# Kernel tuning notes

Measured on AMD Instinct MI355X. Metric: run time of the kernel, lower is better.

## Reference

```python
import jax, jax.numpy as jnp
import numpy as np

NEG = -1e9

def conv1x1(x, w, b):
    # x: [B,C,H,W], w: [O,C], b: [O]
    return jnp.einsum('bchw,oc->bohw', x, w) + b[None, :, None, None]


def setup_inputs() -> dict:
    key = jax.random.key(0)
    ks = jax.random.split(key, 12)
    B, C, H, W = 4, 512, 96, 96
    Cr = min(8, C // 8)  # = 8
    s = lambda fan: 1.0 / np.sqrt(fan)
    inp = {
        'x':   jax.random.normal(ks[0], (B, C, H, W), dtype=jnp.float32),
        'w_h': jax.random.normal(ks[1], (Cr, C), dtype=jnp.float32) * s(C),
        'b_h': jax.random.normal(ks[2], (Cr,), dtype=jnp.float32) * s(C),
        'w_w': jax.random.normal(ks[3], (Cr, C), dtype=jnp.float32) * s(C),
        'b_w': jax.random.normal(ks[4], (Cr,), dtype=jnp.float32) * s(C),
        'w_c': jax.random.normal(ks[5], (C, C), dtype=jnp.float32) * s(C),
        'b_c': jax.random.normal(ks[6], (C,), dtype=jnp.float32) * s(C),
        'w_o': jax.random.normal(ks[7], (C, C), dtype=jnp.float32) * s(C),
        'b_o': jax.random.normal(ks[8], (C,), dtype=jnp.float32) * s(C),
        # alpha/beta/gamma are nn.Parameter(zeros(1)); use small nonzero values
        # so all branches contribute to output/gradients.
        'alpha': jax.random.normal(ks[9], (1,), dtype=jnp.float32) * 0.1,
        'beta':  jax.random.normal(ks[10], (1,), dtype=jnp.float32) * 0.1,
        'gamma': jax.random.normal(ks[11], (1,), dtype=jnp.float32) * 0.1,
    }
    return inp


def reference(x, w_h, b_h, w_w, b_w, w_c, b_c, w_o, b_o, alpha, beta, gamma):
    B, C, H, W = x.shape
    f_hei = conv1x1(x, w_h, b_h)              # [B,Cr,H,W]
    Cr = f_hei.shape[1]
    # Faithful replication of torch permute/contiguous/view sequence
    # (the .view(B*W,-1,H) after permute reinterprets the (H,Cr) layout as (Cr,H)).
    f_h = f_hei.transpose(0, 3, 2, 1).reshape(B * W, Cr, H).transpose(0, 2, 1)  # [B*W,H,Cr]
    f_w = f_hei.transpose(0, 2, 1, 3).reshape(B * H, Cr, W).transpose(0, 2, 1)  # [B*H,W,Cr]
    f_wid = conv1x1(x, w_w, b_w)              # [B,Cr,H,W]
    ff_h = f_wid.transpose(0, 3, 1, 2).reshape(B * W, Cr, H)  # [B*W,Cr,H]
    ff_w = f_wid.transpose(0, 2, 1, 3).reshape(B * H, Cr, W)  # [B*H,Cr,W]
    # channel attention branch
    f_ch = conv1x1(x, w_c, b_c)               # [B,C,H,W]
    f_c = f_ch.reshape(B, C, H * W)           # [B,C,HW]
    ff_c = f_ch.transpose(0, 2, 3, 1).reshape(B, H * W, C)    # [B,HW,C]
    aff_c = jax.nn.softmax(jnp.matmul(f_c, ff_c), axis=2)     # [B,C,C]
    out_C = jnp.matmul(ff_c, aff_c).reshape(B, C, H, W)       # torch .view reinterpretation
    # axial (criss-cross) attention with masked concat-softmax
    E_h = jnp.matmul(f_h, ff_h)               # [B*W,H,H]
    E_h = E_h + (jnp.eye(H, dtype=x.dtype) * NEG)[None, :, :]
    E_h = E_h.reshape(B, W, H, H).transpose(0, 2, 1, 3)       # [B,H,W,H]
    E_w = jnp.matmul(f_w, ff_w).reshape(B, H, W, W)           # [B,H,W,W]
    concate = jax.nn.softmax(jnp.concatenate([E_h, E_w], axis=3), axis=3)  # [B,H,W,H+W]
    h_att = concate[:, :, :, :H].transpose(0, 2, 1, 3).reshape(B * W, H, H)
    w_att = concate[:, :, :, H:].reshape(B * H, W, W)
    f_cha = conv1x1(x, w_o, b_o)              # [B,C,H,W]
    P_H = f_cha.transpose(0, 3, 1, 2).reshape(B * W, C, H)
    P_W = f_cha.transpose(0, 2, 1, 3).reshape(B * H, C, W)
    out_H = jnp.matmul(P_H, h_att.transpose(0, 2, 1)).reshape(B, W, C, H).transpose(0, 2, 3, 1)
    out_W = jnp.matmul(P_W, w_att.transpose(0, 2, 1)).reshape(B, H, C, W).transpose(0, 2, 1, 3)
    return x + alpha * out_H + beta * out_W + gamma * out_C
```

## Files before the change

### kernel.cpp

```cpp
#include <hip/hip_runtime.h>

typedef __attribute__((ext_vector_type(8))) short short8;
typedef __attribute__((ext_vector_type(4))) float f32x4;
typedef __attribute__((ext_vector_type(4))) unsigned short us4;
typedef unsigned short u16;

#define kB 4
#define kC 512
#define kCr 8
#define kH 96
#define kW 96
#define kHW 9216
#define kCHW 4718592
#define NEGV -1e9f

__device__ __forceinline__ u16 f2b(float f) {
  union { float f; unsigned u; } v; v.f = f;
  unsigned r = v.u + 0x7fff + ((v.u >> 16) & 1);
  return (u16)(r >> 16);
}
__device__ __forceinline__ float b2f(u16 h) {
  union { unsigned u; float f; } v; v.u = ((unsigned)h) << 16;
  return v.f;
}
#define MFMA(a, b, c) __builtin_amdgcn_mfma_f32_16x16x32_bf16(a, b, c, 0, 0, 0)

__device__ __forceinline__ void gl16(const u16* g, u16* l) {
  __builtin_amdgcn_global_load_lds(
      (const __attribute__((address_space(1))) void*)g,
      (__attribute__((address_space(3))) void*)l, 16, 0, 0);
}

__global__ __launch_bounds__(256) void k_cvt_T(const float* __restrict__ in,
                                               u16* __restrict__ out,
                                               int R, int C) {
  const float* ib = in + (size_t)blockIdx.z * R * C;
  u16* ob = out + (size_t)blockIdx.z * R * C;
  int c0 = blockIdx.x * 64, r0 = blockIdx.y * 64;
  __shared__ u16 T[64][68];
  int tid = threadIdx.x;
#pragma unroll
  for (int p = 0; p < 4; p++) {
    int ch = tid + p * 256;
    int i = ch >> 4, seg = ch & 15;
    f32x4 v = *(const f32x4*)&ib[(size_t)(r0 + i) * C + c0 + seg * 4];
    T[i][seg*4+0] = f2b(v[0]); T[i][seg*4+1] = f2b(v[1]);
    T[i][seg*4+2] = f2b(v[2]); T[i][seg*4+3] = f2b(v[3]);
  }
  __syncthreads();
#pragma unroll
  for (int p = 0; p < 4; p++) {
    int ch = tid + p * 256;
    int j = ch >> 4, seg = ch & 15;
    us4 o;
#pragma unroll
    for (int e = 0; e < 4; e++) o[e] = T[seg*4+e][j];
    *(us4*)&ob[(size_t)(c0 + j) * R + r0 + seg * 4] = o;
  }
}

__global__ __launch_bounds__(256) void k_cvtw(const float* __restrict__ wc,
                                              const float* __restrict__ wo,
                                              u16* __restrict__ wco) {
  int i = blockIdx.x * 256 + threadIdx.x;
  const float* src = (i < 65536) ? &wc[(size_t)i * 4] : &wo[(size_t)(i - 65536) * 4];
  f32x4 v = *(const f32x4*)src;
  us4 o;
  o[0] = f2b(v[0]); o[1] = f2b(v[1]); o[2] = f2b(v[2]); o[3] = f2b(v[3]);
  ((us4*)wco)[i] = o;
}

__global__ __launch_bounds__(256) void k_conv16(
    const float* __restrict__ wh, const float* __restrict__ bh,
    const float* __restrict__ ww, const float* __restrict__ bw,
    const u16* __restrict__ XT, u16* __restrict__ Out) {
  __shared__ u16 As[16][520];
  __shared__ float bias_s[16];
  int tid = threadIdx.x;
#pragma unroll
  for (int p = 0; p < 4; p++) {
    int ch = tid + p * 256;
    int r = ch >> 6, seg = ch & 63;
    const float* src = (r < 8) ? &wh[r * 512 + seg * 8] : &ww[(r - 8) * 512 + seg * 8];
    f32x4 v0 = *(const f32x4*)src;
    f32x4 v1 = *(const f32x4*)(src + 4);
    short8 sv;
    sv[0]=f2b(v0[0]); sv[1]=f2b(v0[1]); sv[2]=f2b(v0[2]); sv[3]=f2b(v0[3]);
    sv[4]=f2b(v1[0]); sv[5]=f2b(v1[1]); sv[6]=f2b(v1[2]); sv[7]=f2b(v1[3]);
    *(short8*)&As[r][seg * 8] = sv;
  }
  if (tid < 16) bias_s[tid] = (tid < 8) ? bh[tid] : bw[tid - 8];
  __syncthreads();
  int b = blockIdx.y;
  int nb = blockIdx.x * 128 + (tid >> 6) * 32;
  int lane = tid & 63;
  int lr = lane & 15, lg = lane >> 4;
  const u16* Bb = XT + (size_t)b * kCHW;
  f32x4 acc[2] = {};
#pragma unroll 4
  for (int k0 = 0; k0 < 512; k0 += 32) {
    short8 a = *(const short8*)&As[lr][k0 + lg * 8];
    short8 b0 = *(const short8*)&Bb[(size_t)(nb + lr) * 512 + k0 + lg * 8];
    short8 b1 = *(const short8*)&Bb[(size_t)(nb + 16 + lr) * 512 + k0 + lg * 8];
    acc[0] = MFMA(a, b0, acc[0]);
    acc[1] = MFMA(a, b1, acc[1]);
  }
#pragma unroll
  for (int q = 0; q < 2; q++)
#pragma unroll
    for (int r = 0; r < 4; r++) {
      int m = lg * 4 + r;
      Out[((size_t)b * 16 + m) * kHW + nb + q * 16 + lr] = f2b(acc[q][r] + bias_s[m]);
    }
}

#define GEMM_PROLOG()                                                      \
  int tid = threadIdx.x;                                                   \
  int lane = tid & 63, wv = tid >> 6;                                      \
  int wr = (wv >> 1) * 64, wc = (wv & 1) * 64;                             \
  int lr = lane & 15, lg = lane >> 4;                                      \
  f32x4 acc[4][4] = {};

#define STAGE(bufv, kk)                                                    \
  {                                                                        \
    _Pragma("unroll")                                                      \
    for (int p = 0; p < 4; p++) {                                          \
      int ch = tid + p * 256;                                              \
      int row = ch >> 3, cc = ch & 7;                                      \
      int sc = (cc ^ (row & 7)) * 8;                                       \
      gl16(&Asrc[(size_t)(bm + row) * LDA + (kk) + sc], &As[bufv][row][cc * 8]); \
      gl16(&Bsrc[(size_t)(bn + row) * LDB + (kk) + sc], &Bs[bufv][row][cc * 8]); \
    }                                                                      \
  }

#define COMPUTE(bufv)                                                      \
  {                                                                        \
    _Pragma("unroll")                                                      \
    for (int ks = 0; ks < 2; ks++) {                                       \
      int ca = ((ks * 4 + lg) ^ (lr & 7)) * 8;                             \
      short8 av[4], bv[4];                                                 \
      _Pragma("unroll")                                                    \
      for (int m = 0; m < 4; m++)                                          \
        av[m] = *(const short8*)&As[bufv][wr + m * 16 + lr][ca];           \
      _Pragma("unroll")                                                    \
      for (int n = 0; n < 4; n++)                                          \
        bv[n] = *(const short8*)&Bs[bufv][wc + n * 16 + lr][ca];           \
      __builtin_amdgcn_s_setprio(1);                                       \
      _Pragma("unroll")                                                    \
      for (int m = 0; m < 4; m++)                                          \
        _Pragma("unroll")                                                  \
        for (int n = 0; n < 4; n++)                                        \
          acc[m][n] = MFMA(av[m], bv[n], acc[m][n]);                       \
      __builtin_amdgcn_s_setprio(0);                                       \
    }                                                                      \
  }

#define VMBAR(N)                                                           \
  asm volatile("s_waitcnt vmcnt(" #N ")" ::: "memory");                    \
  __builtin_amdgcn_s_barrier();

#define LGBAR                                                              \
  asm volatile("s_waitcnt lgkmcnt(0)" ::: "memory");                       \
  __builtin_amdgcn_s_barrier();

#define PIPELOOP(NT, KBASE)                                                \
  STAGE(0, (KBASE));                                                       \
  STAGE(1, (KBASE) + 64);                                                  \
  {                                                                        \
    int cur = 0;                                                           \
    _Pragma("unroll 1")                                                    \
    for (int t = 0; t < (NT) - 2; t++) {                                   \
      VMBAR(8);                                                            \
      COMPUTE(cur);                                                        \
      LGBAR;                                                               \
      STAGE(cur, (KBASE) + (t + 2) * 64);                                  \
      cur ^= 1;                                                            \
    }                                                                      \
    VMBAR(8);                                                              \
    COMPUTE(cur);                                                          \
    cur ^= 1;                                                              \
    VMBAR(0);                                                              \
    COMPUTE(cur);                                                          \
  }

__global__ __launch_bounds__(256) void k_gemm_conv2(
    const u16* __restrict__ wco, const u16* __restrict__ BT,
    const float* __restrict__ b_c, const float* __restrict__ b_o,
    u16* __restrict__ f_ch, u16* __restrict__ f_cha, u16* __restrict__ f_chT) {
  __shared__ u16 smem[32768];
  u16 (*As)[128][64] = (u16 (*)[128][64])smem;
  u16 (*Bs)[128][64] = (u16 (*)[128][64])(smem + 16384);
  int b = blockIdx.z;
  int bm = blockIdx.y * 128;
  int bn = blockIdx.x * 128;
  const u16* Asrc = wco;
  const u16* Bsrc = BT + (size_t)b * kCHW;
  const int LDA = 512, LDB = 512;
  GEMM_PROLOG();
  PIPELOOP(8, 0);
  const float* biasp = (bm < 512) ? (b_c + bm) : (b_o + bm - 512);
  u16* Ob = (bm < 512) ? (f_ch + (size_t)b * kCHW + (size_t)bm * kHW)
                       : (f_cha + (size_t)b * kCHW + (size_t)(bm - 512) * kHW);
  u16 tvals[4][4];
#pragma unroll
  for (int m = 0; m < 4; m++)
#pragma unroll
    for (int r = 0; r < 4; r++) {
      int ol = wr + m * 16 + lg * 4 + r;
      float bv_ = biasp[ol];
#pragma unroll
      for (int n = 0; n < 4; n++) {
        u16 hv = f2b(acc[m][n][r] + bv_);
        Ob[(size_t)ol * kHW + bn + wc + n * 16 + lr] = hv;
        tvals[m][n] = (r == 0) ? hv : tvals[m][n];
      }
    }
  if (bm < 512) {
    __syncthreads();
    u16 (*T)[136] = (u16 (*)[136])smem;
#pragma unroll
    for (int m = 0; m < 4; m++)
#pragma unroll
      for (int n = 0; n < 4; n++) {
        int ol = wr + m * 16 + lg * 4;
        float bv0 = biasp[ol], bv1 = biasp[ol+1], bv2 = biasp[ol+2], bv3 = biasp[ol+3];
        int nl = wc + n * 16 + lr;
        T[nl][ol + 0] = f2b(acc[m][n][0] + bv0);
        T[nl][ol + 1] = f2b(acc[m][n][1] + bv1);
        T[nl][ol + 2] = f2b(acc[m][n][2] + bv2);
        T[nl][ol + 3] = f2b(acc[m][n][3] + bv3);
      }
    __syncthreads();
    u16* Tb = f_chT + (size_t)b * kCHW;
#pragma unroll
    for (int p = 0; p < 16; p++) {
      int ch = tid + p * 256;
      int row = ch >> 5, seg = ch & 31;
      us4 v = *(const us4*)&T[row][seg * 4];
      *(us4*)&Tb[(size_t)(bn + row) * 512 + bm + seg * 4] = v;
    }
  }
}

__global__ __launch_bounds__(256) void k_gram_sk(const u16* __restrict__ F,
                                                 u16* __restrict__ part) {
  __shared__ u16 As[2][128][64];
  __shared__ u16 Bs[2][128][64];
  int z = blockIdx.z;
  int b = z & 3, s = z >> 2;
  int L = blockIdx.x;
  int bm = (int)((0x3221110000ull >> (4 * L)) & 15) * 128;
  int bn = (int)((0x3323213210ull >> (4 * L)) & 15) * 128;
  const u16* Asrc = F + (size_t)b * kCHW;
  const u16* Bsrc = Asrc;
  const int LDA = kHW, LDB = kHW;
  int kbeg = s * 1152;
  GEMM_PROLOG();
  PIPELOOP(18, kbeg);
  u16* Pb = part + ((size_t)(s * 4 + b)) * 262144;
#pragma unroll
  for (int m = 0; m < 4; m++)
#pragma unroll
    for (int n = 0; n < 4; n++) {
      us4 tv;
#pragma unroll
      for (int r = 0; r < 4; r++) {
        tv[r] = f2b(acc[m][n][r]);
        Pb[(size_t)(bm + wr + m * 16 + lg * 4 + r) * 512 + bn + wc + n * 16 + lr] = tv[r];
      }
      if (bm != bn)
        *(us4*)&Pb[(size_t)(bn + wc + n * 16 + lr) * 512 + bm + wr + m * 16 + lg * 4] = tv;
    }
}

__global__ __launch_bounds__(256) void k_outc(
    const u16* __restrict__ AT, const u16* __restrict__ Bt,
    const float* __restrict__ gamma, u16* __restrict__ Out) {
  __shared__ u16 As[2][128][64];
  __shared__ u16 Bs[2][128][64];
  int b = blockIdx.z;
  int bm = blockIdx.y * 128;
  int bn = blockIdx.x * 128;
  const u16* Asrc = AT + (size_t)b * kCHW;
  const u16* Bsrc = Bt + (size_t)b * 262144;
  const int LDA = 512, LDB = 512;
  GEMM_PROLOG();
  PIPELOOP(8, 0);
  float g = *gamma;
  u16* Ob = Out + (size_t)b * kCHW;
#pragma unroll
  for (int m = 0; m < 4; m++)
#pragma unroll
    for (int r = 0; r < 4; r++) {
      int mm = bm + wr + m * 16 + lg * 4 + r;
#pragma unroll
      for (int n = 0; n < 4; n++)
        Ob[(size_t)mm * 512 + bn + wc + n * 16 + lr] = f2b(g * acc[m][n][r]);
    }
}

__global__ __launch_bounds__(256) void k_softmax512r(const u16* __restrict__ part,
                                                     float* __restrict__ gramN) {
  int b = blockIdx.x >> 9, i = blockIdx.x & 511;
  int tid = threadIdx.x;
  float v0 = 0.f, v1 = 0.f;
#pragma unroll
  for (int s = 0; s < 8; s++) {
    const u16* P = part + ((size_t)(s * 4 + b) * 512 + i) * 512;
    v0 += b2f(P[tid]);
    v1 += b2f(P[tid + 256]);
  }
  int wid = tid >> 6, lane = tid & 63;
  float m = fmaxf(v0, v1);
#pragma unroll
  for (int o = 32; o >= 1; o >>= 1) m = fmaxf(m, __shfl_xor(m, o));
  __shared__ float redm[4], reds[4];
  if (lane == 0) redm[wid] = m;
  __syncthreads();
  m = fmaxf(fmaxf(redm[0], redm[1]), fmaxf(redm[2], redm[3]));
  float e0 = expf(v0 - m), e1 = expf(v1 - m);
  float s = e0 + e1;
#pragma unroll
  for (int o = 32; o >= 1; o >>= 1) s += __shfl_xor(s, o);
  if (lane == 0) reds[wid] = s;
  __syncthreads();
  s = reds[0] + reds[1] + reds[2] + reds[3];
  float inv = 1.0f / s;
  float* R = gramN + ((size_t)b * 512 + i) * 512;
  R[tid] = e0 * inv;
  R[tid + 256] = e1 * inv;
}

__global__ __launch_bounds__(256) void k_eh(
    const u16* __restrict__ fhw, u16* __restrict__ Ccat) {
  int b = blockIdx.x / kW, w = blockIdx.x % kW;
  __shared__ float fh[kH][kCr];
  __shared__ float fw[kCr][kH];
  int tid = threadIdx.x;
  for (int l = tid; l < kH * kCr; l += 256) {
    int i = l >> 3, c = l & 7;
    fh[i][c] = b2f(fhw[((size_t)b * 16 + (i & 7)) * kHW + (c * 12 + (i >> 3)) * kW + w]);
    int c2 = l / kH, j = l % kH;
    fw[c2][j] = b2f(fhw[((size_t)b * 16 + 8 + c2) * kHW + j * kW + w]);
  }
  __syncthreads();
  for (int t = tid; t < kH * kH; t += 256) {
    int i = t / kH, j = t % kH;
    float e = 0.f;
#pragma unroll
    for (int c = 0; c < kCr; c++) e += fh[i][c] * fw[c][j];
    if (i == j) e += NEGV;
    Ccat[(((size_t)b * kH + i) * kW + w) * 192 + j] = f2b(e);
  }
}

__global__ __launch_bounds__(256) void k_ew(
    const u16* __restrict__ fhw, u16* __restrict__ Ccat) {
  int b = blockIdx.x / kH, h = blockIdx.x % kH;
  __shared__ float fh2[kCr][kW];
  __shared__ float fw2[kCr][kW];
  int tid = threadIdx.x;
  for (int l = tid; l < kCr * kW; l += 256) {
    int c = l / kW, w = l % kW;
    fh2[c][w] = b2f(fhw[((size_t)b * 16 + c) * kHW + h * kW + w]);
    fw2[c][w] = b2f(fhw[((size_t)b * 16 + 8 + c) * kHW + h * kW + w]);
  }
  __syncthreads();
  for (int t = tid; t < kW * kW; t += 256) {
    int w = t / kW, j = t % kW;
    float e = 0.f;
#pragma unroll
    for (int c = 0; c < kCr; c++) e += fh2[c][w] * fw2[c][j];
    Ccat[(((size_t)b * kH + h) * kW + w) * 192 + 96 + j] = f2b(e);
  }
}

__global__ __launch_bounds__(256) void k_softmax192(u16* __restrict__ Ccat) {
  int r = blockIdx.x * 4 + (threadIdx.x >> 6);
  int lane = threadIdx.x & 63;
  u16* R = Ccat + (size_t)r * 192;
  float a = b2f(R[lane]), b = b2f(R[lane + 64]), c = b2f(R[lane + 128]);
  float m = fmaxf(a, fmaxf(b, c));
#pragma unroll
  for (int o = 32; o >= 1; o >>= 1) m = fmaxf(m, __shfl_xor(m, o));
  float ea = expf(a - m), eb = expf(b - m), ec = expf(c - m);
  float s = ea + eb + ec;
#pragma unroll
  for (int o = 32; o >= 1; o >>= 1) s += __shfl_xor(s, o);
  float inv = 1.0f / s;
  R[lane] = f2b(ea * inv);
  R[lane + 64] = f2b(eb * inv);
  R[lane + 128] = f2b(ec * inv);
}

__global__ __launch_bounds__(256) void k_tr_plane(const u16* __restrict__ in,
                                                  u16* __restrict__ out) {
  size_t pl = blockIdx.x;
  const u16* ib = in + pl * 9216;
  u16* ob = out + pl * 9216;
  __shared__ u16 T[96][100];
  int tid = threadIdx.x;
  for (int ch = tid; ch < 96 * 24; ch += 256) {
    int i = ch / 24, seg = ch % 24;
    *(us4*)&T[i][seg*4] = *(const us4*)&ib[i*96 + seg*4];
  }
  __syncthreads();
  for (int ch = tid; ch < 96 * 24; ch += 256) {
    int j = ch / 24, seg = ch % 24;
    us4 o;
#pragma unroll
    for (int e = 0; e < 4; e++) o[e] = T[seg*4+e][j];
    *(us4*)&ob[j*96 + seg*4] = o;
  }
}

__global__ __launch_bounds__(512) void k_final_h(
    const u16* __restrict__ AT,
    const u16* __restrict__ att,
    const float* __restrict__ alpha,
    u16* __restrict__ OutHT) {
  int b = blockIdx.x / 96, w = blockIdx.x % 96;
  __shared__ u16 Bs[96][104];
  int tid = threadIdx.x;
  for (int ch = tid; ch < 1152; ch += 512) {
    int h = ch / 12, seg = ch % 12;
    *(short8*)&Bs[h][seg*8] =
        *(const short8*)&att[(((size_t)b*96 + h)*96 + w)*192 + seg*8];
  }
  __syncthreads();
  int lane = tid & 63, wv = tid >> 6;
  int lr = lane & 15, lg = lane >> 4;
  int c0 = wv * 64;
  const u16* Ab = AT + ((size_t)b*512 + c0)*kHW + w*96;
  f32x4 acc[4][6] = {};
#pragma unroll
  for (int ks = 0; ks < 3; ks++) {
    short8 av[4];
#pragma unroll
    for (int m = 0; m < 4; m++)
      av[m] = *(const short8*)&Ab[(size_t)(m*16 + lr)*kHW + ks*32 + lg*8];
#pragma unroll
    for (int n = 0; n < 6; n++) {
      short8 bv = *(const short8*)&Bs[n*16 + lr][ks*32 + lg*8];
#pragma unroll
      for (int m = 0; m < 4; m++) acc[m][n] = MFMA(av[m], bv, acc[m][n]);
    }
  }
  float al = *alpha;
  u16* Ob = OutHT + ((size_t)b*512 + c0)*kHW + w*96;
#pragma unroll
  for (int m = 0; m < 4; m++)
#pragma unroll
    for (int r = 0; r < 4; r++) {
      size_t crow = (size_t)(m*16 + lg*4 + r) * kHW;
#pragma unroll
      for (int n = 0; n < 6; n++)
        Ob[crow + n*16 + lr] = f2b(al * acc[m][n][r]);
    }
}

__global__ __launch_bounds__(512) void k_final_w(
    const u16* __restrict__ A,
    const u16* __restrict__ att,
    const float* __restrict__ beta,
    u16* __restrict__ OutW) {
  int b = blockIdx.x / 96, h = blockIdx.x % 96;
  __shared__ u16 Bs[96][104];
  int tid = threadIdx.x;
  for (int ch = tid; ch < 1152; ch += 512) {
    int wr_ = ch / 12, seg = ch % 12;
    *(short8*)&Bs[wr_][seg*8] =
        *(const short8*)&att[(((size_t)b*96 + h)*96 + wr_)*192 + 96 + seg*8];
  }
  __syncthreads();
  int lane = tid & 63, wv = tid >> 6;
  int lr = lane & 15, lg = lane >> 4;
  int c0 = wv * 64;
  const u16* Ab = A + ((size_t)b*512 + c0)*kHW + h*96;
  f32x4 acc[4][6] = {};
#pragma unroll
  for (int ks = 0; ks < 3; ks++) {
    short8 av[4];
#pragma unroll
    for (int m = 0; m < 4; m++)
      av[m] = *(const short8*)&Ab[(size_t)(m*16 + lr)*kHW + ks*32 + lg*8];
#pragma unroll
    for (int n = 0; n < 6; n++) {
      short8 bv = *(const short8*)&Bs[n*16 + lr][ks*32 + lg*8];
#pragma unroll
      for (int m = 0; m < 4; m++) acc[m][n] = MFMA(av[m], bv, acc[m][n]);
    }
  }
  float be = *beta;
  u16* Ob = OutW + ((size_t)b*512 + c0)*kHW + h*96;
#pragma unroll
  for (int m = 0; m < 4; m++)
#pragma unroll
    for (int r = 0; r < 4; r++) {
      size_t crow = (size_t)(m*16 + lg*4 + r) * kHW;
#pragma unroll
      for (int n = 0; n < 6; n++)
        Ob[crow + n*16 + lr] = f2b(be * acc[m][n][r]);
    }
}

__global__ __launch_bounds__(256) void k_merge(
    const float* __restrict__ x, const u16* __restrict__ OutC,
    const u16* __restrict__ OutW, const u16* __restrict__ HT,
    float* __restrict__ out) {
  size_t pl = blockIdx.x;
  const u16* hb = HT + pl * 9216;
  __shared__ u16 T[96][100];
  int tid = threadIdx.x;
  for (int ch = tid; ch < 96 * 24; ch += 256) {
    int i = ch / 24, seg = ch % 24;
    *(us4*)&T[i][seg*4] = *(const us4*)&hb[i*96 + seg*4];
  }
  __syncthreads();
  const float* xb = x + pl * 9216;
  const u16* cb = OutC + pl * 9216;
  const u16* wb = OutW + pl * 9216;
  float* ob = out + pl * 9216;
  for (int ch = tid; ch < 2304; ch += 256) {
    int i4 = ch * 4;
    int h = i4 / 96, w = i4 % 96;
    f32x4 xv = *(const f32x4*)&xb[i4];
    us4 cv = *(const us4*)&cb[i4];
    us4 wv = *(const us4*)&wb[i4];
    f32x4 o;
#pragma unroll
    for (int e = 0; e < 4; e++)
      o[e] = xv[e] + b2f(cv[e]) + b2f(wv[e]) + b2f(T[w + e][h]);
    *(f32x4*)&ob[i4] = o;
  }
}

extern "C" void kernel_launch(void* const* d_in, const int* in_sizes, int n_in,
                              void* d_out, int out_size, void* d_ws, size_t ws_size,
                              hipStream_t stream) {
  const float* x     = (const float*)d_in[0];
  const float* w_h   = (const float*)d_in[1];
  const float* b_h   = (const float*)d_in[2];
  const float* w_w   = (const float*)d_in[3];
  const float* b_w   = (const float*)d_in[4];
  const float* w_c   = (const float*)d_in[5];
  const float* b_c   = (const float*)d_in[6];
  const float* w_o   = (const float*)d_in[7];
  const float* b_o   = (const float*)d_in[8];
  const float* alpha = (const float*)d_in[9];
  const float* beta  = (const float*)d_in[10];
  const float* gamma = (const float*)d_in[11];
  float* out = (float*)d_out;

  const size_t R = 37748736;
  char* p = (char*)d_ws;
  u16*   xbfT   = (u16*)(p);
  u16*   part   = (u16*)(p);
  u16*   f_chaT = (u16*)(p);
  u16*   outW   = (u16*)(p);
  u16*   f_ch   = (u16*)(p + R);
  u16*   outC   = (u16*)(p + R);
  u16*   f_chT  = (u16*)(p + 2 * R);
  u16*   outHT  = (u16*)(p + 2 * R);
  u16*   f_cha  = (u16*)(p + 3 * R);
  u16*   fhw    = (u16*)(p + 4 * R);
  char*  F      = p + 4 * R + 2359296;
  float* gramN  = (float*)F;
  u16*   affT   = (u16*)(F + 4194304);
  u16*   ccat   = (u16*)F;
  u16*   wco    = (u16*)(F + 14155776);

  k_cvt_T<<<dim3(144, 8, 4), 256, 0, stream>>>(x, xbfT, 512, 9216);
  k_cvtw<<<512, 256, 0, stream>>>(w_c, w_o, wco);
  k_conv16<<<dim3(72, 4), 256, 0, stream>>>(w_h, b_h, w_w, b_w, xbfT, fhw);
  k_gemm_conv2<<<dim3(72, 8, 4), 256, 0, stream>>>(wco, xbfT, b_c, b_o, f_ch, f_cha, f_chT);
  k_gram_sk<<<dim3(10, 1, 32), 256, 0, stream>>>(f_ch, part);
  k_softmax512r<<<2048, 256, 0, stream>>>(part, gramN);
  k_cvt_T<<<dim3(8, 8, 4), 256, 0, stream>>>(gramN, affT, 512, 512);
  k_outc<<<dim3(4, 72, 4), 256, 0, stream>>>(f_chT, affT, gamma, outC);
  k_eh<<<384, 256, 0, stream>>>(fhw, ccat);
  k_ew<<<384, 256, 0, stream>>>(fhw, ccat);
  k_softmax192<<<9216, 256, 0, stream>>>(ccat);
  k_tr_plane<<<2048, 256, 0, stream>>>(f_cha, f_chaT);
  k_final_h<<<384, 512, 0, stream>>>(f_chaT, ccat, alpha, outHT);
  k_final_w<<<384, 512, 0, stream>>>(f_cha, ccat, beta, outW);
  k_merge<<<2048, 256, 0, stream>>>(x, outC, outW, outHT, out);
}
```

Measured before the change: 294.0 us.

## Replace conv GEMM with 256x256-tile, 8-wave kernel using phased LDS reads

Replaces the 128x128 tile, 4-wave conv GEMM (w_c/w_o stacked times x) with a 256x256 tile, 8-wave kernel. The new kernel double-buffers LDS, splits each K-step into four phases separated by barriers, and raises wave priority around the MFMA groups. Larger tiles raise arithmetic intensity and cut global reloads. The trade-off is 128 KB of LDS, a high accumulator register count, and only 576 blocks. The transposed f_chT write-out is done in two passes to fit the staging buffer.

```diff
diff --git a/kernel.cpp b/kernel.cpp
--- a/kernel.cpp
+++ b/kernel.cpp
@@ -112,6 +112,135 @@
       int m = lg * 4 + r;
       Out[((size_t)b * 16 + m) * kHW + nb + q * 16 + lr] = f2b(acc[q][r] + bias_s[m]);
     }
+}
+
+__global__ __launch_bounds__(512) void k_conv2_8ph(
+    const u16* __restrict__ wco, const u16* __restrict__ BT,
+    const float* __restrict__ b_c, const float* __restrict__ b_o,
+    u16* __restrict__ f_ch, u16* __restrict__ f_cha, u16* __restrict__ f_chT) {
+  __shared__ u16 smem[65536];
+  int tid = threadIdx.x;
+  int lane = tid & 63, wid = tid >> 6;
+  int wm = wid >> 2, wn = wid & 3;
+  int lr = lane & 15, lg = lane >> 4;
+  int b = blockIdx.z;
+  int bm = blockIdx.y * 256;
+  int bn = blockIdx.x * 256;
+  const u16* Asrc = wco;
+  const u16* Bsrc = BT + (size_t)b * kCHW;
+  f32x4 acc[8][4] = {};
+  short8 av[4], bv[4];
+
+#define STG8(bf, kt)                                                         \
+  {                                                                          \
+    u16* base_ = smem + (bf) * 32768;                                        \
+    _Pragma("unroll")                                                        \
+    for (int p = 0; p < 4; p++) {                                            \
+      int ch = tid + p * 512;                                                \
+      int row = ch >> 3, cc = ch & 7;                                        \
+      int sc = (cc ^ (row & 7)) * 8;                                         \
+      gl16(&Asrc[(size_t)(bm + row) * 512 + (kt) * 64 + sc], base_ + ch * 8);\
+      gl16(&Bsrc[(size_t)(bn + row) * 512 + (kt) * 64 + sc],                 \
+           base_ + 16384 + ch * 8);                                          \
+    }                                                                        \
+  }
+
+#define RD_B(bf, ks)                                                         \
+  {                                                                          \
+    const u16* Bb_ = smem + (bf) * 32768 + 16384;                            \
+    int ca_ = (((ks) * 4 + lg) ^ (lr & 7)) * 8;                              \
+    _Pragma("unroll")                                                        \
+    for (int n = 0; n < 4; n++)                                              \
+      bv[n] = *(const short8*)&Bb_[(wn * 64 + n * 16 + lr) * 64 + ca_];      \
+  }
+
+#define RD_A(bf, mq, ks)                                                     \
+  {                                                                          \
+    const u16* Ab_ = smem + (bf) * 32768;                                    \
+    int ca_ = (((ks) * 4 + lg) ^ (lr & 7)) * 8;                              \
+    _Pragma("unroll")                                                        \
+    for (int j = 0; j < 4; j++)                                              \
+      av[j] = *(const short8*)&Ab_[(wm * 128 + ((mq) * 4 + j) * 16 + lr) * 64 + ca_];\
+  }
+
+#define MM16(mq)                                                             \
+  __builtin_amdgcn_s_setprio(1);                                             \
+  _Pragma("unroll")                                                          \
+  for (int j = 0; j < 4; j++)                                                \
+    _Pragma("unroll")                                                        \
+    for (int n = 0; n < 4; n++)                                              \
+      acc[(mq) * 4 + j][n] = MFMA(av[j], bv[n], acc[(mq) * 4 + j][n]);       \
+  __builtin_amdgcn_s_setprio(0);
+
+#define PBAR asm volatile("s_barrier" ::: "memory");
+#define GATE asm volatile("s_waitcnt vmcnt(0)" ::: "memory"); PBAR
+
+  STG8(0, 0);
+  GATE;
+#pragma unroll 1
+  for (int kt = 0; kt < 8; kt++) {
+    int bf = kt & 1;
+    if (kt < 7) STG8(bf ^ 1, kt + 1);
+    RD_B(bf, 0); RD_A(bf, 0, 0); MM16(0); PBAR;
+    RD_A(bf, 1, 0); MM16(1); PBAR;
+    RD_B(bf, 1); RD_A(bf, 0, 1); MM16(0); PBAR;
+    RD_A(bf, 1, 1); MM16(1);
+    GATE;
+  }
+
+  const float* biasp = (bm < 512) ? (b_c + bm) : (b_o + bm - 512);
+  u16* Ob = (bm < 512) ? (f_ch + (size_t)b * kCHW + (size_t)bm * kHW)
+                       : (f_cha + (size_t)b * kCHW + (size_t)(bm - 512) * kHW);
+  float biasr[32];
+#pragma unroll
+  for (int m = 0; m < 8; m++)
+#pragma unroll
+    for (int r = 0; r < 4; r++)
+      biasr[m * 4 + r] = biasp[wm * 128 + m * 16 + lg * 4 + r];
+#pragma unroll
+  for (int m = 0; m < 8; m++)
+#pragma unroll
+    for (int r = 0; r < 4; r++) {
+      int ol = wm * 128 + m * 16 + lg * 4 + r;
+#pragma unroll
+      for (int n = 0; n < 4; n++)
+        Ob[(size_t)ol * kHW + bn + wn * 64 + n * 16 + lr] =
+            f2b(acc[m][n][r] + biasr[m * 4 + r]);
+    }
+  if (bm < 512) {
+    u16* Tb = f_chT + (size_t)b * kCHW;
+    u16 (*T)[264] = (u16 (*)[264])smem;
+#pragma unroll 1
+    for (int pass = 0; pass < 2; pass++) {
+      __syncthreads();
+      if ((wn >> 1) == pass) {
+        int hb_ = wn & 1;
+#pragma unroll
+        for (int m = 0; m < 8; m++)
+#pragma unroll
+          for (int n = 0; n < 4; n++) {
+            int hwl = hb_ * 64 + n * 16 + lr;
+            int ol = wm * 128 + m * 16 + lg * 4;
+            us4 tv;
+#pragma unroll
+            for (int r = 0; r < 4; r++) tv[r] = f2b(acc[m][n][r] + biasr[m * 4 + r]);
+            *(us4*)&T[hwl][ol] = tv;
+          }
+      }
+      __syncthreads();
+#pragma unroll
+      for (int p = 0; p < 16; p++) {
+        int ch = tid + p * 512;
+        int row = ch >> 6, seg = ch & 63;
+        us4 v = *(const us4*)&T[row][seg * 4];
+        *(us4*)&Tb[(size_t)(bn + pass * 128 + row) * 512 + bm + seg * 4] = v;
+      }
+    }
+  }
+#undef STG8
+#undef RD_B
+#undef RD_A
+#undef MM16
 }
 
 #define GEMM_PROLOG()                                                      \
@@ -183,65 +312,6 @@
     COMPUTE(cur);                                                          \
   }
 
-__global__ __launch_bounds__(256) void k_gemm_conv2(
-    const u16* __restrict__ wco, const u16* __restrict__ BT,
-    const float* __restrict__ b_c, const float* __restrict__ b_o,
-    u16* __restrict__ f_ch, u16* __restrict__ f_cha, u16* __restrict__ f_chT) {
-  __shared__ u16 smem[32768];
-  u16 (*As)[128][64] = (u16 (*)[128][64])smem;
-  u16 (*Bs)[128][64] = (u16 (*)[128][64])(smem + 16384);
-  int b = blockIdx.z;
-  int bm = blockIdx.y * 128;
-  int bn = blockIdx.x * 128;
-  const u16* Asrc = wco;
-  const u16* Bsrc = BT + (size_t)b * kCHW;
-  const int LDA = 512, LDB = 512;
-  GEMM_PROLOG();
-  PIPELOOP(8, 0);
-  const float* biasp = (bm < 512) ? (b_c + bm) : (b_o + bm - 512);
-  u16* Ob = (bm < 512) ? (f_ch + (size_t)b * kCHW + (size_t)bm * kHW)
-                       : (f_cha + (size_t)b * kCHW + (size_t)(bm - 512) * kHW);
-  u16 tvals[4][4];
-#pragma unroll
-  for (int m = 0; m < 4; m++)
-#pragma unroll
-    for (int r = 0; r < 4; r++) {
-      int ol = wr + m * 16 + lg * 4 + r;
-      float bv_ = biasp[ol];
-#pragma unroll
-      for (int n = 0; n < 4; n++) {
-        u16 hv = f2b(acc[m][n][r] + bv_);
-        Ob[(size_t)ol * kHW + bn + wc + n * 16 + lr] = hv;
-        tvals[m][n] = (r == 0) ? hv : tvals[m][n];
-      }
-    }
-  if (bm < 512) {
-    __syncthreads();
-    u16 (*T)[136] = (u16 (*)[136])smem;
-#pragma unroll
-    for (int m = 0; m < 4; m++)
-#pragma unroll
-      for (int n = 0; n < 4; n++) {
-        int ol = wr + m * 16 + lg * 4;
-        float bv0 = biasp[ol], bv1 = biasp[ol+1], bv2 = biasp[ol+2], bv3 = biasp[ol+3];
-        int nl = wc + n * 16 + lr;
-        T[nl][ol + 0] = f2b(acc[m][n][0] + bv0);
-        T[nl][ol + 1] = f2b(acc[m][n][1] + bv1);
-        T[nl][ol + 2] = f2b(acc[m][n][2] + bv2);
-        T[nl][ol + 3] = f2b(acc[m][n][3] + bv3);
-      }
-    __syncthreads();
-    u16* Tb = f_chT + (size_t)b * kCHW;
-#pragma unroll
-    for (int p = 0; p < 16; p++) {
-      int ch = tid + p * 256;
-      int row = ch >> 5, seg = ch & 31;
-      us4 v = *(const us4*)&T[row][seg * 4];
-      *(us4*)&Tb[(size_t)(bn + row) * 512 + bm + seg * 4] = v;
-    }
-  }
-}
-
 __global__ __launch_bounds__(256) void k_gram_sk(const u16* __restrict__ F,
                                                  u16* __restrict__ part) {
   __shared__ u16 As[2][128][64];
@@ -573,7 +643,7 @@
   k_cvt_T<<<dim3(144, 8, 4), 256, 0, stream>>>(x, xbfT, 512, 9216);
   k_cvtw<<<512, 256, 0, stream>>>(w_c, w_o, wco);
   k_conv16<<<dim3(72, 4), 256, 0, stream>>>(w_h, b_h, w_w, b_w, xbfT, fhw);
-  k_gemm_conv2<<<dim3(72, 8, 4), 256, 0, stream>>>(wco, xbfT, b_c, b_o, f_ch, f_cha, f_chT);
+  k_conv2_8ph<<<dim3(36, 4, 4), 512, 0, stream>>>(wco, xbfT, b_c, b_o, f_ch, f_cha, f_chT);
   k_gram_sk<<<dim3(10, 1, 32), 256, 0, stream>>>(f_ch, part);
   k_softmax512r<<<2048, 256, 0, stream>>>(part, gramN);
   k_cvt_T<<<dim3(8, 8, 4), 256, 0, stream>>>(gramN, affT, 512, 512);
```

After: 298.5 us. About the same (+1.5%).

## Compute two N-tiles per block in conv GEMM with a continuous pipeline

Applied to the files above, without the earlier changes.

The 1x1-conv GEMM kernel now computes two adjacent 128-column output tiles per block, using two accumulator sets. One double-buffered load pipeline runs across both tiles, so the second tile's loads overlap the first tile's tail and there is one prolog per pair. The grid is halved along N. Bias values are loaded once into registers and the transposed stores are packed as 4-element vectors. This doubles accumulator register use, which may lower occupancy, and leaves fewer blocks to spread across the compute units.

```diff
diff --git a/kernel.cpp b/kernel.cpp
--- a/kernel.cpp
+++ b/kernel.cpp
@@ -133,7 +133,7 @@
     }                                                                      \
   }
 
-#define COMPUTE(bufv)                                                      \
+#define COMPUTE_T(bufv, ACC)                                               \
   {                                                                        \
     _Pragma("unroll")                                                      \
     for (int ks = 0; ks < 2; ks++) {                                       \
@@ -150,10 +150,12 @@
       for (int m = 0; m < 4; m++)                                          \
         _Pragma("unroll")                                                  \
         for (int n = 0; n < 4; n++)                                        \
-          acc[m][n] = MFMA(av[m], bv[n], acc[m][n]);                       \
+          ACC[m][n] = MFMA(av[m], bv[n], ACC[m][n]);                       \
       __builtin_amdgcn_s_setprio(0);                                       \
     }                                                                      \
   }
+
+#define COMPUTE(bufv) COMPUTE_T(bufv, acc)
 
 #define VMBAR(N)                                                           \
   asm volatile("s_waitcnt vmcnt(" #N ")" ::: "memory");                    \
@@ -190,56 +192,108 @@
   __shared__ u16 smem[32768];
   u16 (*As)[128][64] = (u16 (*)[128][64])smem;
   u16 (*Bs)[128][64] = (u16 (*)[128][64])(smem + 16384);
+  int tid = threadIdx.x;
+  int lane = tid & 63, wv = tid >> 6;
+  int wr = (wv >> 1) * 64, wc = (wv & 1) * 64;
+  int lr = lane & 15, lg = lane >> 4;
   int b = blockIdx.z;
   int bm = blockIdx.y * 128;
-  int bn = blockIdx.x * 128;
+  int bn0 = blockIdx.x * 256;
   const u16* Asrc = wco;
   const u16* Bsrc = BT + (size_t)b * kCHW;
-  const int LDA = 512, LDB = 512;
-  GEMM_PROLOG();
-  PIPELOOP(8, 0);
+  f32x4 acc0[4][4] = {};
+  f32x4 acc1[4][4] = {};
+
+#define F_STG(bufv, g)                                                     \
+  {                                                                        \
+    int kk_ = ((g) & 7) * 64;                                              \
+    int bn_ = bn0 + (((g) >> 3) & 1) * 128;                                \
+    _Pragma("unroll")                                                      \
+    for (int p = 0; p < 4; p++) {                                          \
+      int ch = tid + p * 256;                                              \
+      int row = ch >> 3, cc = ch & 7;                                      \
+      int sc = (cc ^ (row & 7)) * 8;                                       \
+      gl16(&Asrc[(size_t)(bm + row) * 512 + kk_ + sc], &As[bufv][row][cc * 8]); \
+      gl16(&Bsrc[(size_t)(bn_ + row) * 512 + kk_ + sc], &Bs[bufv][row][cc * 8]); \
+    }                                                                      \
+  }
+
+  F_STG(0, 0);
+  F_STG(1, 1);
+  int cur = 0;
+#pragma unroll 1
+  for (int t = 0; t < 8; t++) {
+    VMBAR(8);
+    COMPUTE_T(cur, acc0);
+    LGBAR;
+    F_STG(cur, t + 2);
+    cur ^= 1;
+  }
+#pragma unroll 1
+  for (int t = 8; t < 14; t++) {
+    VMBAR(8);
+    COMPUTE_T(cur, acc1);
+    LGBAR;
+    F_STG(cur, t + 2);
+    cur ^= 1;
+  }
+  VMBAR(8);
+  COMPUTE_T(cur, acc1);
+  cur ^= 1;
+  VMBAR(0);
+  COMPUTE_T(cur, acc1);
+
   const float* biasp = (bm < 512) ? (b_c + bm) : (b_o + bm - 512);
   u16* Ob = (bm < 512) ? (f_ch + (size_t)b * kCHW + (size_t)bm * kHW)
                        : (f_cha + (size_t)b * kCHW + (size_t)(bm - 512) * kHW);
-  u16 tvals[4][4];
+  float biasr[16];
+#pragma unroll
+  for (int m = 0; m < 4; m++)
+#pragma unroll
+    for (int r = 0; r < 4; r++)
+      biasr[m * 4 + r] = biasp[wr + m * 16 + lg * 4 + r];
 #pragma unroll
   for (int m = 0; m < 4; m++)
 #pragma unroll
     for (int r = 0; r < 4; r++) {
       int ol = wr + m * 16 + lg * 4 + r;
-      float bv_ = biasp[ol];
+      float bv_ = biasr[m * 4 + r];
 #pragma unroll
       for (int n = 0; n < 4; n++) {
-        u16 hv = f2b(acc[m][n][r] + bv_);
-        Ob[(size_t)ol * kHW + bn + wc + n * 16 + lr] = hv;
-        tvals[m][n] = (r == 0) ? hv : tvals[m][n];
+        Ob[(size_t)ol * kHW + bn0 + wc + n * 16 + lr] = f2b(acc0[m][n][r] + bv_);
+        Ob[(size_t)ol * kHW + bn0 + 128 + wc + n * 16 + lr] = f2b(acc1[m][n][r] + bv_);
       }
     }
   if (bm < 512) {
-    __syncthreads();
+    u16* Tb = f_chT + (size_t)b * kCHW;
     u16 (*T)[136] = (u16 (*)[136])smem;
-#pragma unroll
-    for (int m = 0; m < 4; m++)
-#pragma unroll
-      for (int n = 0; n < 4; n++) {
-        int ol = wr + m * 16 + lg * 4;
-        float bv0 = biasp[ol], bv1 = biasp[ol+1], bv2 = biasp[ol+2], bv3 = biasp[ol+3];
-        int nl = wc + n * 16 + lr;
-        T[nl][ol + 0] = f2b(acc[m][n][0] + bv0);
-        T[nl][ol + 1] = f2b(acc[m][n][1] + bv1);
-        T[nl][ol + 2] = f2b(acc[m][n][2] + bv2);
-        T[nl][ol + 3] = f2b(acc[m][n][3] + bv3);
+#pragma unroll 1
+    for (int s = 0; s < 2; s++) {
+      __syncthreads();
+#pragma unroll
+      for (int m = 0; m < 4; m++)
+#pragma unroll
+        for (int n = 0; n < 4; n++) {
+          int ol = wr + m * 16 + lg * 4;
+          int nl = wc + n * 16 + lr;
+          us4 tv;
+#pragma unroll
+          for (int r = 0; r < 4; r++)
+            tv[r] = f2b((s ? acc1[m][n][r] : acc0[m][n][r]) + biasr[m * 4 + r]);
+          *(us4*)&T[nl][ol] = tv;
+        }
+      __syncthreads();
+      int bn_ = bn0 + s * 128;
+#pragma unroll
+      for (int p = 0; p < 16; p++) {
+        int ch = tid + p * 256;
+        int row = ch >> 5, seg = ch & 31;
+        us4 v = *(const us4*)&T[row][seg * 4];
+        *(us4*)&Tb[(size_t)(bn_ + row) * 512 + bm + seg * 4] = v;
       }
-    __syncthreads();
-    u16* Tb = f_chT + (size_t)b * kCHW;
-#pragma unroll
-    for (int p = 0; p < 16; p++) {
-      int ch = tid + p * 256;
-      int row = ch >> 5, seg = ch & 31;
-      us4 v = *(const us4*)&T[row][seg * 4];
-      *(us4*)&Tb[(size_t)(bn + row) * 512 + bm + seg * 4] = v;
-    }
-  }
+    }
+  }
+#undef F_STG
 }
 
 __global__ __launch_bounds__(256) void k_gram_sk(const u16* __restrict__ F,
@@ -573,7 +627,7 @@
   k_cvt_T<<<dim3(144, 8, 4), 256, 0, stream>>>(x, xbfT, 512, 9216);
   k_cvtw<<<512, 256, 0, stream>>>(w_c, w_o, wco);
   k_conv16<<<dim3(72, 4), 256, 0, stream>>>(w_h, b_h, w_w, b_w, xbfT, fhw);
-  k_gemm_conv2<<<dim3(72, 8, 4), 256, 0, stream>>>(wco, xbfT, b_c, b_o, f_ch, f_cha, f_chT);
+  k_gemm_conv2<<<dim3(36, 8, 4), 256, 0, stream>>>(wco, xbfT, b_c, b_o, f_ch, f_cha, f_chT);
   k_gram_sk<<<dim3(10, 1, 32), 256, 0, stream>>>(f_ch, part);
   k_softmax512r<<<2048, 256, 0, stream>>>(part, gramN);
   k_cvt_T<<<dim3(8, 8, 4), 256, 0, stream>>>(gramN, affT, 512, 512);
```

New measurement: 318.4 us. 8.3% more time.
